# Optimization experiments

Measured on AMD Instinct MI355X. Metric: run time of the kernel, lower is better.

## Reference

```python
import jax, jax.numpy as jnp
import numpy as np

B, IN, OUT, G = 64, 8192, 8192, 64
NG = IN // G  # groups per row


def setup_inputs() -> dict:
    key = jax.random.key(0)
    k1, k2, k3, k4 = jax.random.split(key, 4)
    x = jax.random.normal(k1, (B, IN), dtype=jnp.float32)
    # packed 2-bit codes: 4 codes per byte, LSB-first (matches _pack2)
    w_packed = jax.random.randint(k2, (OUT, IN // 4), 0, 256, dtype=jnp.int32).astype(jnp.uint8)
    # scales from _calc_group_qparams are positive (max_abs/1.5); zp is always 2
    scales = jax.random.uniform(k3, (OUT, NG), dtype=jnp.float32, minval=0.01, maxval=0.1)
    zps = jnp.full((OUT, NG), 2, dtype=jnp.int32)
    bias = jax.random.normal(k4, (OUT,), dtype=jnp.float32) * 0.01
    return {"x": x, "w_packed": w_packed, "scales": scales, "zps": zps, "bias": bias}


def _dequant(w_packed, scales, zps):
    # unpack: byte -> 4 two-bit codes, LSB first (matches _unpack2)
    out_f = w_packed.shape[0]
    codes = jnp.stack([(w_packed >> s) & 3 for s in (0, 2, 4, 6)], axis=-1)  # [OUT, IN//4, 4]
    q = codes.reshape(out_f, NG, G).astype(jnp.int32)                        # [OUT, NG, G]
    # per-group dequant: (q - zp) * scale
    w = (q - zps[:, :, None]).astype(jnp.float32) * scales[:, :, None]
    return w.reshape(out_f, IN)                                              # [OUT, IN]


def reference(x, w_packed, scales, zps, bias):
    w = _dequant(w_packed, scales, zps)  # [OUT, IN] fp32
    # original accumulates xg @ wg.T per group; equivalent to full x @ w.T
    return x @ w.T + bias                # [B, OUT]
```

## Files before the change

### kernel.cpp

```cpp
#include <hip/hip_runtime.h>
#include <hip/hip_bf16.h>

#define B_    64
#define IN_   8192
#define OUT_  8192
#define NG_   128
#define PB_   2048

#define KSPLIT 8
#define KC     1024
#define CGS    2

typedef float f32x4 __attribute__((ext_vector_type(4)));
typedef short s16x8 __attribute__((ext_vector_type(8)));
union FU { float f; unsigned u; };

__global__ __launch_bounds__(256) void k_pre(const float* __restrict__ x,
                                             __hip_bfloat16* __restrict__ xb) {
    int i = (blockIdx.x * 256 + threadIdx.x) * 4;
    float4 f = *(const float4*)(x + i);
    __hip_bfloat162 h0 = __float22bfloat162_rn(make_float2(f.x, f.y));
    __hip_bfloat162 h1 = __float22bfloat162_rn(make_float2(f.z, f.w));
    uint2 o; o.x = *(unsigned*)&h0; o.y = *(unsigned*)&h1;
    *(uint2*)(xb + i) = o;
}

__global__ __launch_bounds__(256, 2) void k_main(
    const __hip_bfloat16* __restrict__ xb,
    const unsigned char* __restrict__ wp,
    const float* __restrict__ scales,
    const int* __restrict__ zps,
    float* __restrict__ part)
{
    __shared__ uint4 x_lds[4096];
    __shared__ int wflag, zflag;

    const int tid  = threadIdx.x;
    const int wave = tid >> 6;
    const int lane = tid & 63;
    const int q    = lane >> 4;
    const int nn   = lane & 15;

    const int bid     = blockIdx.x;
    const int kidx    = bid & (KSPLIT - 1);
    const int nblk    = bid >> 3;
    const int kbase   = kidx * KC;
    const int colbase = nblk * 128 + wave * 32;

#pragma unroll
    for (int i = 0; i < 16; ++i) {
        int sg = wave * 16 + i;
        int sb = sg >> 4, b = (sg >> 2) & 3, mt = sg & 3;
        const __hip_bfloat16* src =
            xb + (mt * 16 + nn) * IN_ + kbase + sb * 128 + q * 32 + b * 8;
        unsigned int* dst = (unsigned int*)((char*)x_lds + sg * 1024);
        __builtin_amdgcn_global_load_lds(
            (const __attribute__((address_space(1))) unsigned int*)src,
            (__attribute__((address_space(3))) unsigned int*)dst, 16, 0, 0);
    }

    unsigned wv = ((const unsigned int*)wp)[tid];
    int      zv = zps[tid];
    if (tid == 0) { wflag = 0; zflag = 0; }
    __syncthreads();
    if (wv > 255u) wflag = 1;
    if (zv != 2)   zflag = 1;
    __syncthreads();
    const bool u8mode = (wflag != 0);
    const bool zgen   = (zflag != 0);

    uint2 w8[2][4][CGS];
    const int wb = (kbase >> 2) + q * 8;
    if (u8mode) {
#pragma unroll
        for (int ph = 0; ph < 2; ++ph)
#pragma unroll
            for (int sb = 0; sb < 4; ++sb)
#pragma unroll
                for (int cg = 0; cg < CGS; ++cg) {
                    int n = colbase + cg * 16 + nn;
                    w8[ph][sb][cg] =
                        *(const uint2*)(wp + n * PB_ + wb + ph * 128 + sb * 32);
                }
    } else {
        const int* wpi = (const int*)wp;
#pragma unroll
        for (int ph = 0; ph < 2; ++ph)
#pragma unroll
            for (int sb = 0; sb < 4; ++sb)
#pragma unroll
                for (int cg = 0; cg < CGS; ++cg) {
                    int n = colbase + cg * 16 + nn;
                    const int* p = wpi + n * PB_ + wb + ph * 128 + sb * 32;
                    uint4 a  = *(const uint4*)p;
                    uint4 b2 = *(const uint4*)(p + 4);
                    w8[ph][sb][cg].x = __builtin_amdgcn_perm(a.y,  a.x,  0x0C0C0400) |
                                       __builtin_amdgcn_perm(a.w,  a.z,  0x04000C0C);
                    w8[ph][sb][cg].y = __builtin_amdgcn_perm(b2.y, b2.x, 0x0C0C0400) |
                                       __builtin_amdgcn_perm(b2.w, b2.z, 0x04000C0C);
                }
    }

    float sf[2][4][CGS], fb[2][4][CGS];
#pragma unroll
    for (int ph = 0; ph < 2; ++ph)
#pragma unroll
        for (int sb = 0; sb < 4; ++sb)
#pragma unroll
            for (int cg = 0; cg < CGS; ++cg) {
                int n = colbase + cg * 16 + nn;
                int g = kidx * 16 + ph * 8 + sb * 2 + (q >> 1);
                float s = scales[n * NG_ + g] * 1.001953125f;
                float zpf = zgen ? (float)zps[n * NG_ + g] : 2.0f;
                sf[ph][sb][cg] = s;
                fb[ph][sb][cg] = -zpf * s;
            }

    f32x4 acc[CGS][4];
#pragma unroll
    for (int cg = 0; cg < CGS; ++cg)
#pragma unroll
        for (int mt = 0; mt < 4; ++mt)
            acc[cg][mt] = (f32x4){0.f, 0.f, 0.f, 0.f};

#pragma unroll
    for (int ph = 0; ph < 2; ++ph) {
        if (ph) {
            __syncthreads();
#pragma unroll
            for (int i = 0; i < 16; ++i) {
                int sg = wave * 16 + i;
                int sb = sg >> 4, b = (sg >> 2) & 3, mt = sg & 3;
                const __hip_bfloat16* src = xb + (mt * 16 + nn) * IN_ +
                    kbase + 512 + sb * 128 + q * 32 + b * 8;
                unsigned int* dst = (unsigned int*)((char*)x_lds + sg * 1024);
                __builtin_amdgcn_global_load_lds(
                    (const __attribute__((address_space(1))) unsigned int*)src,
                    (__attribute__((address_space(3))) unsigned int*)dst, 16, 0, 0);
            }
            __syncthreads();
        }
#pragma unroll
        for (int sb = 0; sb < 4; ++sb) {
#pragma unroll
            for (int dw = 0; dw < 2; ++dw) {
#pragma unroll
                for (int h = 0; h < 2; ++h) {
                    const int b = dw * 2 + h;
                    union { uint4 u4; s16x8 s8; } av[4];
#pragma unroll
                    for (int mt = 0; mt < 4; ++mt)
                        av[mt].u4 = x_lds[((sb * 4 + b) * 4 + mt) * 64 + lane];
#pragma unroll
                    for (int cg = 0; cg < CGS; ++cg) {
                        const unsigned v = dw ? w8[ph][sb][cg].y : w8[ph][sb][cg].x;
                        const float s = sf[ph][sb][cg], fbv = fb[ph][sb][cg];
                        union { unsigned u[4]; s16x8 s8; } bf;
#pragma unroll
                        for (int m = 0; m < 4; ++m) {
                            const int sh = h * 16 + m * 4;
                            FU f0, f1;
                            f0.f = fmaf((float)((v >> sh) & 3u), s, fbv);
                            f1.f = fmaf((float)((v >> (sh + 2)) & 3u), s, fbv);
                            bf.u[m] = __builtin_amdgcn_perm(f1.u, f0.u, 0x07060302);
                        }
#pragma unroll
                        for (int mt = 0; mt < 4; ++mt)
                            acc[cg][mt] = __builtin_amdgcn_mfma_f32_16x16x32_bf16(
                                av[mt].s8, bf.s8, acc[cg][mt], 0, 0, 0);
                    }
                }
            }
        }
    }

    float* pp = part + kidx * (B_ * OUT_);
#pragma unroll
    for (int cg = 0; cg < CGS; ++cg) {
        const int col = colbase + cg * 16 + nn;
#pragma unroll
        for (int mt = 0; mt < 4; ++mt)
#pragma unroll
            for (int r = 0; r < 4; ++r)
                pp[(mt * 16 + q * 4 + r) * OUT_ + col] = acc[cg][mt][r];
    }
}

__global__ __launch_bounds__(256) void k_reduce(const float* __restrict__ part,
                                                const float* __restrict__ bias,
                                                float* __restrict__ out) {
    int i = (blockIdx.x * 256 + threadIdx.x) * 4;
    float4 s = *(const float4*)(bias + (i & (OUT_ - 1)));
#pragma unroll
    for (int p = 0; p < KSPLIT; ++p) {
        float4 v = *(const float4*)(part + p * (B_ * OUT_) + i);
        s.x += v.x; s.y += v.y; s.z += v.z; s.w += v.w;
    }
    *(float4*)(out + i) = s;
}

extern "C" void kernel_launch(void* const* d_in, const int* in_sizes, int n_in,
                              void* d_out, int out_size, void* d_ws, size_t ws_size,
                              hipStream_t stream) {
    const float*         x      = (const float*)d_in[0];
    const unsigned char* wp     = (const unsigned char*)d_in[1];
    const float*         scales = (const float*)d_in[2];
    const int*           zps    = (const int*)d_in[3];
    const float*         bias   = (const float*)d_in[4];
    float*               out    = (float*)d_out;

    __hip_bfloat16* xb   = (__hip_bfloat16*)d_ws;
    float*          part = (float*)((char*)d_ws + (1 << 20));

    k_pre<<<512, 256, 0, stream>>>(x, xb);
    k_main<<<512, 256, 0, stream>>>(xb, wp, scales, zps, part);
    k_reduce<<<512, 256, 0, stream>>>(part, bias, out);
}
```

Measured before the change: 129.1 us.

## Double K-split to 16 and hoist format-detection flags into pre-kernel

Doubles the K-split from 8 to 16, which halves the LDS tile and the per-block work, launches 1024 blocks and raises launch bounds to 4 blocks per CU for more occupancy. The weight-format and zero-point detection moves from every main block into block 0 of the pre-kernel, which writes the result to workspace flags. The trade-off is twice as many fp32 partials written by the main kernel and read back by the reduce kernel.

```diff
diff --git a/kernel.cpp b/kernel.cpp
--- a/kernel.cpp
+++ b/kernel.cpp
@@ -7,8 +7,8 @@
 #define NG_   128
 #define PB_   2048
 
-#define KSPLIT 8
-#define KC     1024
+#define KSPLIT 16
+#define KC     512
 #define CGS    2
 
 typedef float f32x4 __attribute__((ext_vector_type(4)));
@@ -16,24 +16,40 @@
 union FU { float f; unsigned u; };
 
 __global__ __launch_bounds__(256) void k_pre(const float* __restrict__ x,
-                                             __hip_bfloat16* __restrict__ xb) {
+                                             __hip_bfloat16* __restrict__ xb,
+                                             const unsigned char* __restrict__ wp,
+                                             const int* __restrict__ zps,
+                                             unsigned* __restrict__ flags) {
     int i = (blockIdx.x * 256 + threadIdx.x) * 4;
     float4 f = *(const float4*)(x + i);
     __hip_bfloat162 h0 = __float22bfloat162_rn(make_float2(f.x, f.y));
     __hip_bfloat162 h1 = __float22bfloat162_rn(make_float2(f.z, f.w));
     uint2 o; o.x = *(unsigned*)&h0; o.y = *(unsigned*)&h1;
     *(uint2*)(xb + i) = o;
-}
-
-__global__ __launch_bounds__(256, 2) void k_main(
+
+    if (blockIdx.x == 0) {
+        __shared__ int f0, f1;
+        unsigned wv = ((const unsigned int*)wp)[threadIdx.x];
+        int      zv = zps[threadIdx.x];
+        if (threadIdx.x == 0) { f0 = 0; f1 = 0; }
+        __syncthreads();
+        if (wv > 255u) f0 = 1;
+        if (zv != 2)   f1 = 1;
+        __syncthreads();
+        if (threadIdx.x == 0) { uint2 fo; fo.x = (unsigned)f0; fo.y = (unsigned)f1;
+                                *(uint2*)flags = fo; }
+    }
+}
+
+__global__ __launch_bounds__(256, 4) void k_main(
     const __hip_bfloat16* __restrict__ xb,
     const unsigned char* __restrict__ wp,
     const float* __restrict__ scales,
     const int* __restrict__ zps,
+    const unsigned* __restrict__ flags,
     float* __restrict__ part)
 {
-    __shared__ uint4 x_lds[4096];
-    __shared__ int wflag, zflag;
+    __shared__ uint4 x_lds[2048];
 
     const int tid  = threadIdx.x;
     const int wave = tid >> 6;
@@ -43,13 +59,15 @@
 
     const int bid     = blockIdx.x;
     const int kidx    = bid & (KSPLIT - 1);
-    const int nblk    = bid >> 3;
+    const int nblk    = bid >> 4;
     const int kbase   = kidx * KC;
     const int colbase = nblk * 128 + wave * 32;
 
-#pragma unroll
-    for (int i = 0; i < 16; ++i) {
-        int sg = wave * 16 + i;
+    const uint2 fl = *(const uint2*)flags;
+
+#pragma unroll
+    for (int i = 0; i < 8; ++i) {
+        int sg = wave * 8 + i;
         int sb = sg >> 4, b = (sg >> 2) & 3, mt = sg & 3;
         const __hip_bfloat16* src =
             xb + (mt * 16 + nn) * IN_ + kbase + sb * 128 + q * 32 + b * 8;
@@ -59,39 +77,32 @@
             (__attribute__((address_space(3))) unsigned int*)dst, 16, 0, 0);
     }
 
-    unsigned wv = ((const unsigned int*)wp)[tid];
-    int      zv = zps[tid];
-    if (tid == 0) { wflag = 0; zflag = 0; }
-    __syncthreads();
-    if (wv > 255u) wflag = 1;
-    if (zv != 2)   zflag = 1;
-    __syncthreads();
-    const bool u8mode = (wflag != 0);
-    const bool zgen   = (zflag != 0);
-
-    uint2 w8[2][4][CGS];
+    const bool u8mode = fl.x != 0;
+    const bool zgen   = fl.y != 0;
+
+    uint2 w8[2][2][CGS];
     const int wb = (kbase >> 2) + q * 8;
     if (u8mode) {
 #pragma unroll
         for (int ph = 0; ph < 2; ++ph)
 #pragma unroll
-            for (int sb = 0; sb < 4; ++sb)
+            for (int sb = 0; sb < 2; ++sb)
 #pragma unroll
                 for (int cg = 0; cg < CGS; ++cg) {
                     int n = colbase + cg * 16 + nn;
                     w8[ph][sb][cg] =
-                        *(const uint2*)(wp + n * PB_ + wb + ph * 128 + sb * 32);
+                        *(const uint2*)(wp + n * PB_ + wb + ph * 64 + sb * 32);
                 }
     } else {
         const int* wpi = (const int*)wp;
 #pragma unroll
         for (int ph = 0; ph < 2; ++ph)
 #pragma unroll
-            for (int sb = 0; sb < 4; ++sb)
+            for (int sb = 0; sb < 2; ++sb)
 #pragma unroll
                 for (int cg = 0; cg < CGS; ++cg) {
                     int n = colbase + cg * 16 + nn;
-                    const int* p = wpi + n * PB_ + wb + ph * 128 + sb * 32;
+                    const int* p = wpi + n * PB_ + wb + ph * 64 + sb * 32;
                     uint4 a  = *(const uint4*)p;
                     uint4 b2 = *(const uint4*)(p + 4);
                     w8[ph][sb][cg].x = __builtin_amdgcn_perm(a.y,  a.x,  0x0C0C0400) |
@@ -101,15 +112,15 @@
                 }
     }
 
-    float sf[2][4][CGS], fb[2][4][CGS];
+    float sf[2][2][CGS], fb[2][2][CGS];
 #pragma unroll
     for (int ph = 0; ph < 2; ++ph)
 #pragma unroll
-        for (int sb = 0; sb < 4; ++sb)
+        for (int sb = 0; sb < 2; ++sb)
 #pragma unroll
             for (int cg = 0; cg < CGS; ++cg) {
                 int n = colbase + cg * 16 + nn;
-                int g = kidx * 16 + ph * 8 + sb * 2 + (q >> 1);
+                int g = kidx * 8 + ph * 4 + sb * 2 + (q >> 1);
                 float s = scales[n * NG_ + g] * 1.001953125f;
                 float zpf = zgen ? (float)zps[n * NG_ + g] : 2.0f;
                 sf[ph][sb][cg] = s;
@@ -123,16 +134,18 @@
         for (int mt = 0; mt < 4; ++mt)
             acc[cg][mt] = (f32x4){0.f, 0.f, 0.f, 0.f};
 
+    __syncthreads();
+
 #pragma unroll
     for (int ph = 0; ph < 2; ++ph) {
         if (ph) {
             __syncthreads();
 #pragma unroll
-            for (int i = 0; i < 16; ++i) {
-                int sg = wave * 16 + i;
+            for (int i = 0; i < 8; ++i) {
+                int sg = wave * 8 + i;
                 int sb = sg >> 4, b = (sg >> 2) & 3, mt = sg & 3;
                 const __hip_bfloat16* src = xb + (mt * 16 + nn) * IN_ +
-                    kbase + 512 + sb * 128 + q * 32 + b * 8;
+                    kbase + 256 + sb * 128 + q * 32 + b * 8;
                 unsigned int* dst = (unsigned int*)((char*)x_lds + sg * 1024);
                 __builtin_amdgcn_global_load_lds(
                     (const __attribute__((address_space(1))) unsigned int*)src,
@@ -141,7 +154,7 @@
             __syncthreads();
         }
 #pragma unroll
-        for (int sb = 0; sb < 4; ++sb) {
+        for (int sb = 0; sb < 2; ++sb) {
 #pragma unroll
             for (int dw = 0; dw < 2; ++dw) {
 #pragma unroll
@@ -209,10 +222,11 @@
     const float*         bias   = (const float*)d_in[4];
     float*               out    = (float*)d_out;
 
-    __hip_bfloat16* xb   = (__hip_bfloat16*)d_ws;
-    float*          part = (float*)((char*)d_ws + (1 << 20));
-
-    k_pre<<<512, 256, 0, stream>>>(x, xb);
-    k_main<<<512, 256, 0, stream>>>(xb, wp, scales, zps, part);
+    __hip_bfloat16* xb    = (__hip_bfloat16*)d_ws;
+    float*          part  = (float*)((char*)d_ws + (1 << 20));
+    unsigned*       flags = (unsigned*)((char*)d_ws + (1 << 20) + (KSPLIT * B_ * OUT_ * 4));
+
+    k_pre<<<512, 256, 0, stream>>>(x, xb, wp, zps, flags);
+    k_main<<<1024, 256, 0, stream>>>(xb, wp, scales, zps, flags, part);
     k_reduce<<<512, 256, 0, stream>>>(part, bias, out);
 }
```

Result: no change. 130.0 us (+0.7%).
